# Performance work log

Measured on AMD Instinct MI355X. Metric: run time of the kernel, lower is better.

Reference implementation:

```python
import jax, jax.numpy as jnp
import numpy as np

LN_EPS = 1e-5


def setup_inputs() -> dict:
    key = jax.random.key(0)
    ks = jax.random.split(key, 4)
    B, L, Dm, N = 16, 2048, 512, 64
    return {
        "x": jax.random.normal(ks[0], (B, L, Dm), dtype=jnp.float32),
        "A": jax.random.normal(ks[1], (Dm, N), dtype=jnp.float32),
        "C": jax.random.normal(ks[2], (Dm, N), dtype=jnp.float32),
        "D": jax.random.normal(ks[3], (Dm,), dtype=jnp.float32),
        "gamma": jnp.ones((Dm,), dtype=jnp.float32),
        "beta": jnp.zeros((Dm,), dtype=jnp.float32),
    }


def reference(x, A, C, D, gamma, beta):
    # LayerNorm over last dim (matches nn.LayerNorm(d_model))
    mean = jnp.mean(x, axis=-1, keepdims=True)
    var = jnp.mean(jnp.square(x - mean), axis=-1, keepdims=True)
    x_norm = (x - mean) * jax.lax.rsqrt(var + LN_EPS) * gamma + beta

    B, L, Dm = x.shape
    N = A.shape[1]
    h0 = jnp.zeros((B, N), dtype=x.dtype)

    def step(h, u):
        # u: [B, Dm]; h: [B, N]
        h = jnp.tanh(u @ A + h)
        y = h @ C.T + u * D  # [B, Dm]
        return h, y

    # scan over time: xs [L, B, Dm]
    _, ys = jax.lax.scan(step, h0, jnp.swapaxes(x_norm, 0, 1))
    out = jnp.swapaxes(ys, 0, 1)  # [B, L, Dm]
    return out + x
```

## Files before the change

### kernel.cpp

```cpp
#include <hip/hip_runtime.h>
#include <hip/hip_bf16.h>

typedef short bf16x8 __attribute__((ext_vector_type(8)));
typedef float f32x4 __attribute__((ext_vector_type(4)));

constexpr int B_ = 16;
constexpr int L_ = 2048;
constexpr int DM = 512;
constexpr int NS = 64;
constexpr int BL = B_ * L_;
constexpr float LN_EPS = 1e-5f;
constexpr float KLN = 2.8853900817779268f;

constexpr int SEGS = 32;
constexpr int LSEG = L_ / SEGS;
constexpr int WARM = 64;

__device__ __forceinline__ unsigned f32bits(float f) {
    union { float f; unsigned u; } v{f}; return v.u;
}
__device__ __forceinline__ float bitsf32(unsigned u) {
    union { unsigned u; float f; } v{u}; return v.f;
}
__device__ __forceinline__ unsigned short f2bf(float f) {
    unsigned u = f32bits(f);
    unsigned r = u + 0x7FFF + ((u >> 16) & 1);
    return (unsigned short)(r >> 16);
}

__device__ __forceinline__ void norm_split8(float4 u0, float4 u1,
                                            float rstd, float m2,
                                            bf16x8& ah, bf16x8& al) {
    float t[8] = { fmaf(u0.x, rstd, m2), fmaf(u0.y, rstd, m2),
                   fmaf(u0.z, rstd, m2), fmaf(u0.w, rstd, m2),
                   fmaf(u1.x, rstd, m2), fmaf(u1.y, rstd, m2),
                   fmaf(u1.z, rstd, m2), fmaf(u1.w, rstd, m2) };
    unsigned hb[8], lb[8];
    #pragma unroll
    for (int j = 0; j < 8; ++j) {
        unsigned tb = f32bits(t[j]);
        hb[j] = tb & 0xFFFF0000u;
        lb[j] = f32bits(t[j] - bitsf32(hb[j]));
    }
    union { unsigned u[4]; bf16x8 v; } H, L;
    #pragma unroll
    for (int p = 0; p < 4; ++p) {
        H.u[p] = (hb[2*p] >> 16) | hb[2*p+1];
        L.u[p] = (lb[2*p] >> 16) | (lb[2*p+1] & 0xFFFF0000u);
    }
    ah = H.v; al = L.v;
}

__global__ __launch_bounds__(256) void k_pack(const float* __restrict__ A,
                                              const float* __restrict__ C,
                                              const float* __restrict__ gamma,
                                              const float* __restrict__ beta,
                                              const float* __restrict__ Dv,
                                              unsigned short* __restrict__ PAh,
                                              unsigned short* __restrict__ PAl,
                                              unsigned short* __restrict__ PC,
                                              float* __restrict__ c0,
                                              float* __restrict__ gd,
                                              float* __restrict__ bd) {
    const int blk = blockIdx.x;
    const int tid = threadIdx.x;
    if (blk < 32) {
        const int g = blk * 256 + tid;
        if (g < 4096) {
            const int lane = g & 63, ct = (g >> 6) & 3, k32 = (g >> 8) & 3, kc = g >> 10;
            const int kbase = kc * 128 + k32 * 32 + (lane >> 4) * 8;
            const int col   = ct * 16 + (lane & 15);
            unsigned hb[8], lb[8];
            #pragma unroll
            for (int j = 0; j < 8; ++j) {
                float v = gamma[kbase + j] * A[(size_t)(kbase + j) * NS + col];
                unsigned tb = f32bits(v);
                hb[j] = tb & 0xFFFF0000u;
                lb[j] = f32bits(v - bitsf32(hb[j]));
            }
            uint4 ph, pl;
            ph.x = (hb[0] >> 16) | hb[1]; ph.y = (hb[2] >> 16) | hb[3];
            ph.z = (hb[4] >> 16) | hb[5]; ph.w = (hb[6] >> 16) | hb[7];
            pl.x = (lb[0] >> 16) | (lb[1] & 0xFFFF0000u);
            pl.y = (lb[2] >> 16) | (lb[3] & 0xFFFF0000u);
            pl.z = (lb[4] >> 16) | (lb[5] & 0xFFFF0000u);
            pl.w = (lb[6] >> 16) | (lb[7] & 0xFFFF0000u);
            *reinterpret_cast<uint4*>(PAh + (size_t)g * 8) = ph;
            *reinterpret_cast<uint4*>(PAl + (size_t)g * 8) = pl;
        } else {
            const int g2 = g - 4096;
            const int d = g2 >> 3, s = g2 & 7;
            const int nbase = (s ^ (d & 7)) * 8;
            unsigned short v[8];
            #pragma unroll
            for (int j = 0; j < 8; ++j) v[j] = f2bf(C[(size_t)d * NS + nbase + j]);
            uint4 p;
            p.x = v[0] | ((unsigned)v[1] << 16); p.y = v[2] | ((unsigned)v[3] << 16);
            p.z = v[4] | ((unsigned)v[5] << 16); p.w = v[6] | ((unsigned)v[7] << 16);
            *reinterpret_cast<uint4*>(PC + (size_t)g2 * 8) = p;
        }
    } else {
        __shared__ float red[256];
        #pragma unroll
        for (int i = 0; i < 2; ++i) {
            int d = tid + 256 * i;
            gd[d] = gamma[d] * Dv[d];
            bd[d] = beta[d] * Dv[d];
        }
        const int n = tid & 63, part = tid >> 6;
        float s = 0.f;
        #pragma unroll 8
        for (int k = part * 128; k < part * 128 + 128; ++k)
            s += beta[k] * A[(size_t)k * NS + n];
        red[tid] = s;
        __syncthreads();
        if (tid < 64)
            c0[tid] = red[tid] + red[tid + 64] + red[tid + 128] + red[tid + 192];
    }
}

__global__ __launch_bounds__(256) void k_gemmA(const float* __restrict__ x,
                                               const unsigned short* __restrict__ PAh,
                                               const unsigned short* __restrict__ PAl,
                                               const float* __restrict__ c0,
                                               float* __restrict__ stats,
                                               float* __restrict__ Bu) {
    __shared__ unsigned short AsH[4 * 4 * 64 * 8];
    __shared__ unsigned short AsL[4 * 4 * 64 * 8];
    const int tid  = threadIdx.x;
    const int r0   = blockIdx.x * 64;
    const int w    = tid >> 6;
    const int lane = tid & 63;
    const int myrow = 16 * w + (lane & 15);
    const int kb    = (lane >> 4) * 8;
    const float* xrow = x + (size_t)(r0 + myrow) * DM;

    float s = 0.f, s2 = 0.f;
    #pragma unroll
    for (int kc = 0; kc < 4; ++kc) {
        #pragma unroll
        for (int k32 = 0; k32 < 4; ++k32) {
            float4 a = *reinterpret_cast<const float4*>(xrow + kc * 128 + k32 * 32 + kb);
            float4 b = *reinterpret_cast<const float4*>(xrow + kc * 128 + k32 * 32 + kb + 4);
            s  += (a.x + a.y) + (a.z + a.w) + (b.x + b.y) + (b.z + b.w);
            s2 += a.x*a.x + a.y*a.y + a.z*a.z + a.w*a.w
                + b.x*b.x + b.y*b.y + b.z*b.z + b.w*b.w;
        }
    }
    s += __shfl_xor(s, 16); s2 += __shfl_xor(s2, 16);
    s += __shfl_xor(s, 32); s2 += __shfl_xor(s2, 32);
    const float mean = s * (1.0f / DM);
    const float var  = s2 * (1.0f / DM) - mean * mean;
    const float rstd = rsqrtf(var + LN_EPS);
    const float m2   = -mean * rstd;
    if (lane < 16) {
        stats[2 * (r0 + myrow)]     = mean;
        stats[2 * (r0 + myrow) + 1] = rstd;
    }

    f32x4 acc[4] = {};
    const bf16x8* ABh = reinterpret_cast<const bf16x8*>(AsH);
    const bf16x8* ABl = reinterpret_cast<const bf16x8*>(AsL);

    float4 xv[8];
    #pragma unroll
    for (int k32 = 0; k32 < 4; ++k32) {
        xv[2*k32]   = *reinterpret_cast<const float4*>(xrow + k32 * 32 + kb);
        xv[2*k32+1] = *reinterpret_cast<const float4*>(xrow + k32 * 32 + kb + 4);
    }

    for (int kc = 0; kc < 4; ++kc) {
        {
            const float4* sh = reinterpret_cast<const float4*>(PAh + (size_t)kc * 8192);
            const float4* sl = reinterpret_cast<const float4*>(PAl + (size_t)kc * 8192);
            float4* dh = reinterpret_cast<float4*>(AsH);
            float4* dl = reinterpret_cast<float4*>(AsL);
            #pragma unroll
            for (int i = 0; i < 4; ++i) {
                dh[tid + 256 * i] = sh[tid + 256 * i];
                dl[tid + 256 * i] = sl[tid + 256 * i];
            }
        }
        float4 nxt[8];
        if (kc < 3) {
            #pragma unroll
            for (int k32 = 0; k32 < 4; ++k32) {
                nxt[2*k32]   = *reinterpret_cast<const float4*>(
                    xrow + (kc + 1) * 128 + k32 * 32 + kb);
                nxt[2*k32+1] = *reinterpret_cast<const float4*>(
                    xrow + (kc + 1) * 128 + k32 * 32 + kb + 4);
            }
        }
        __syncthreads();
        #pragma unroll
        for (int k32 = 0; k32 < 4; ++k32) {
            bf16x8 ah, al;
            norm_split8(xv[2*k32], xv[2*k32+1], rstd, m2, ah, al);
            #pragma unroll
            for (int ct = 0; ct < 4; ++ct) {
                bf16x8 bh = ABh[(k32 * 4 + ct) * 64 + lane];
                bf16x8 bl = ABl[(k32 * 4 + ct) * 64 + lane];
                acc[ct] = __builtin_amdgcn_mfma_f32_16x16x32_bf16(ah, bh, acc[ct], 0, 0, 0);
                acc[ct] = __builtin_amdgcn_mfma_f32_16x16x32_bf16(ah, bl, acc[ct], 0, 0, 0);
                acc[ct] = __builtin_amdgcn_mfma_f32_16x16x32_bf16(al, bh, acc[ct], 0, 0, 0);
            }
        }
        __syncthreads();
        if (kc < 3) {
            #pragma unroll
            for (int i = 0; i < 8; ++i) xv[i] = nxt[i];
        }
    }

    const int orow = r0 + 16 * w + (lane >> 4) * 4;
    #pragma unroll
    for (int ct = 0; ct < 4; ++ct) {
        const int n = ct * 16 + (lane & 15);
        const float c0n = c0[n];
        #pragma unroll
        for (int j = 0; j < 4; ++j)
            Bu[(size_t)(orow + j) * NS + n] = acc[ct][j] + c0n;
    }
}

__global__ __launch_bounds__(64) void k_scan(const float* __restrict__ Bu,
                                             unsigned short* __restrict__ h) {
    constexpr int G = 16;
    const int seg = blockIdx.x & (SEGS - 1);
    const int b   = blockIdx.x / SEGS;
    const int n   = threadIdx.x;
    const int l0     = seg * LSEG;
    const int start  = (seg == 0) ? 0 : (l0 - WARM);
    const int nGrp   = (l0 + LSEG - start) / G;
    const int gStore = (l0 - start) / G;

    const float* bp = Bu + (size_t)b * L_ * NS + n;
    unsigned short* hp = h + (size_t)b * L_ * NS + n;

    float bufA[G], bufB[G];
    #pragma unroll
    for (int j = 0; j < G; ++j) bufA[j] = KLN * bp[(size_t)(start + j) * NS];

    float hv = 0.0f;
    int g = 0;
    for (;;) {
        {
            const int base = start + (g + 1) * G;
            if (g + 1 < nGrp) {
                #pragma unroll
                for (int j = 0; j < G; ++j)
                    bufB[j] = KLN * bp[(size_t)(base + j) * NS];
            }
            unsigned short* hq = hp + (size_t)(start + g * G) * NS;
            const bool doStore = g >= gStore;
            #pragma unroll
            for (int j = 0; j < G; ++j) {
                float t = fmaf(hv, KLN, bufA[j]);
                float e = __builtin_amdgcn_exp2f(t);
                float rr = __builtin_amdgcn_rcpf(e + 1.0f);
                hv = fmaf(-2.0f, rr, 1.0f);
                if (doStore) hq[(size_t)j * NS] = f2bf(hv);
            }
        }
        if (++g == nGrp) break;
        {
            const int base = start + (g + 1) * G;
            if (g + 1 < nGrp) {
                #pragma unroll
                for (int j = 0; j < G; ++j)
                    bufA[j] = KLN * bp[(size_t)(base + j) * NS];
            }
            unsigned short* hq = hp + (size_t)(start + g * G) * NS;
            const bool doStore = g >= gStore;
            #pragma unroll
            for (int j = 0; j < G; ++j) {
                float t = fmaf(hv, KLN, bufB[j]);
                float e = __builtin_amdgcn_exp2f(t);
                float rr = __builtin_amdgcn_rcpf(e + 1.0f);
                hv = fmaf(-2.0f, rr, 1.0f);
                if (doStore) hq[(size_t)j * NS] = f2bf(hv);
            }
        }
        if (++g == nGrp) break;
    }
}

__global__ __launch_bounds__(256) void k_gemmC(const float* __restrict__ x,
                                               const unsigned short* __restrict__ PC,
                                               const float* __restrict__ gd,
                                               const float* __restrict__ bd,
                                               const float* __restrict__ stats,
                                               const unsigned short* __restrict__ h,
                                               float* __restrict__ out) {
    __shared__ unsigned short Hs[64 * 64];
    __shared__ unsigned short Cs[128 * 64];
    const int tid  = threadIdx.x;
    const int r0   = (blockIdx.x >> 2) * 64;
    const int d0   = (blockIdx.x & 3) * 128;
    const int w    = tid >> 6;
    const int lane = tid & 63;

    {
        const float4* src = reinterpret_cast<const float4*>(PC + (size_t)d0 * NS);
        float4* dst = reinterpret_cast<float4*>(Cs);
        #pragma unroll
        for (int i = 0; i < 4; ++i) dst[tid + 256 * i] = src[tid + 256 * i];
    }
    {
        const char* hb = reinterpret_cast<const char*>(h + (size_t)r0 * NS);
        #pragma unroll
        for (int it = 0; it < 2; ++it) {
            const int o   = it * 4096 + tid * 16;
            const int row = o >> 7;
            const int s   = (o >> 4) & 7;
            uint4 v = *reinterpret_cast<const uint4*>(hb + row * 128 + ((s ^ (row & 7)) << 4));
            *reinterpret_cast<uint4*>(reinterpret_cast<char*>(Hs) + o) = v;
        }
    }
    __syncthreads();

    f32x4 acc[8] = {};
    const int arow = 16 * w + (lane & 15);
    #pragma unroll
    for (int kt = 0; kt < 2; ++kt) {
        const int c = kt * 4 + (lane >> 4);
        bf16x8 a = *reinterpret_cast<const bf16x8*>(
            reinterpret_cast<char*>(Hs) + arow * 128 + ((c ^ (arow & 7)) << 4));
        #pragma unroll
        for (int ct = 0; ct < 8; ++ct) {
            const int dl = ct * 16 + (lane & 15);
            bf16x8 bfr = *reinterpret_cast<const bf16x8*>(
                reinterpret_cast<char*>(Cs) + dl * 128 + ((c ^ (dl & 7)) << 4));
            acc[ct] = __builtin_amdgcn_mfma_f32_16x16x32_bf16(a, bfr, acc[ct], 0, 0, 0);
        }
    }

    const int rbase = r0 + 16 * w + (lane >> 4) * 4;
    float mean_[4], rstd_[4];
    #pragma unroll
    for (int j = 0; j < 4; ++j) {
        mean_[j] = stats[2 * (rbase + j)];
        rstd_[j] = stats[2 * (rbase + j) + 1];
    }
    #pragma unroll
    for (int ct = 0; ct < 8; ++ct) {
        const int d  = d0 + ct * 16 + (lane & 15);
        const float gdv = gd[d];
        const float bdv = bd[d];
        #pragma unroll
        for (int j = 0; j < 4; ++j) {
            const size_t idx = (size_t)(rbase + j) * DM + d;
            const float xv = x[idx];
            const float z  = (xv - mean_[j]) * rstd_[j];
            out[idx] = acc[ct][j] + z * gdv + bdv + xv;
        }
    }
}

extern "C" void kernel_launch(void* const* d_in, const int* in_sizes, int n_in,
                              void* d_out, int out_size, void* d_ws, size_t ws_size,
                              hipStream_t stream) {
    const float* x     = (const float*)d_in[0];
    const float* A     = (const float*)d_in[1];
    const float* C     = (const float*)d_in[2];
    const float* Dv    = (const float*)d_in[3];
    const float* gamma = (const float*)d_in[4];
    const float* beta  = (const float*)d_in[5];
    float* out = (float*)d_out;

    char* ws = (char*)d_ws;
    float* Bu           = (float*)(ws);
    unsigned short* h   = (unsigned short*)(ws + (size_t)BL * NS * 4);
    float* stats        = (float*)(ws + (size_t)BL * NS * 6);
    char* p = ws + (size_t)BL * NS * 6 + (size_t)BL * 2 * 4;
    unsigned short* PAh = (unsigned short*)p;            p += (size_t)DM * NS * 2;
    unsigned short* PAl = (unsigned short*)p;            p += (size_t)DM * NS * 2;
    unsigned short* PC  = (unsigned short*)p;            p += (size_t)DM * NS * 2;
    float* c0           = (float*)p;                     p += 256;
    float* gd           = (float*)p;                     p += (size_t)DM * 4;
    float* bd           = (float*)p;

    k_pack<<<33, 256, 0, stream>>>(A, C, gamma, beta, Dv, PAh, PAl, PC, c0, gd, bd);
    k_gemmA<<<BL / 64, 256, 0, stream>>>(x, PAh, PAl, c0, stats, Bu);
    k_scan<<<B_ * SEGS, 64, 0, stream>>>(Bu, h);
    k_gemmC<<<(BL / 64) * (DM / 128), 256, 0, stream>>>(x, PC, gd, bd, stats, h, out);
}
```

Measured before the change: 78.00 us.

## Load full projection matrix into LDS once and keep whole x row in registers

The A-projection GEMM kernel now uses 512-thread blocks covering 128 rows. The whole packed hi/lo A matrix (128 KB) is staged in shared memory once up front instead of being reloaded per k-chunk with two barriers each. Each thread also holds its entire row slice of x in registers, so x is read once for both the LayerNorm stats and the MFMA operands rather than twice. This removes redundant global traffic and per-chunk synchronisation, but the large LDS footprint and 128 float registers for x may limit occupancy (launch bounds ask for 2 blocks per CU) and remove any load/compute overlap.

After: 73.75 us. 1.06x faster.

```diff
diff --git a/kernel.cpp b/kernel.cpp
--- a/kernel.cpp
+++ b/kernel.cpp
@@ -119,33 +119,52 @@
     }
 }
 
-__global__ __launch_bounds__(256) void k_gemmA(const float* __restrict__ x,
+__global__ __launch_bounds__(512, 2) void k_gemmA(const float* __restrict__ x,
                                                const unsigned short* __restrict__ PAh,
                                                const unsigned short* __restrict__ PAl,
                                                const float* __restrict__ c0,
                                                float* __restrict__ stats,
                                                float* __restrict__ Bu) {
-    __shared__ unsigned short AsH[4 * 4 * 64 * 8];
-    __shared__ unsigned short AsL[4 * 4 * 64 * 8];
+    __shared__ unsigned short AsH[4 * 16 * 64 * 8];
+    __shared__ unsigned short AsL[4 * 16 * 64 * 8];
     const int tid  = threadIdx.x;
-    const int r0   = blockIdx.x * 64;
+    const int r0   = blockIdx.x * 128;
     const int w    = tid >> 6;
     const int lane = tid & 63;
     const int myrow = 16 * w + (lane & 15);
     const int kb    = (lane >> 4) * 8;
     const float* xrow = x + (size_t)(r0 + myrow) * DM;
 
+    {
+        const float4* sh = reinterpret_cast<const float4*>(PAh);
+        const float4* sl = reinterpret_cast<const float4*>(PAl);
+        float4* dh = reinterpret_cast<float4*>(AsH);
+        float4* dl = reinterpret_cast<float4*>(AsL);
+        #pragma unroll
+        for (int i = 0; i < 8; ++i) {
+            dh[tid + 512 * i] = sh[tid + 512 * i];
+            dl[tid + 512 * i] = sl[tid + 512 * i];
+        }
+    }
+
+    float4 xv[32];
+    #pragma unroll
+    for (int kc = 0; kc < 4; ++kc) {
+        #pragma unroll
+        for (int k32 = 0; k32 < 4; ++k32) {
+            xv[kc * 8 + 2 * k32]     = *reinterpret_cast<const float4*>(
+                xrow + kc * 128 + k32 * 32 + kb);
+            xv[kc * 8 + 2 * k32 + 1] = *reinterpret_cast<const float4*>(
+                xrow + kc * 128 + k32 * 32 + kb + 4);
+        }
+    }
+
     float s = 0.f, s2 = 0.f;
     #pragma unroll
-    for (int kc = 0; kc < 4; ++kc) {
-        #pragma unroll
-        for (int k32 = 0; k32 < 4; ++k32) {
-            float4 a = *reinterpret_cast<const float4*>(xrow + kc * 128 + k32 * 32 + kb);
-            float4 b = *reinterpret_cast<const float4*>(xrow + kc * 128 + k32 * 32 + kb + 4);
-            s  += (a.x + a.y) + (a.z + a.w) + (b.x + b.y) + (b.z + b.w);
-            s2 += a.x*a.x + a.y*a.y + a.z*a.z + a.w*a.w
-                + b.x*b.x + b.y*b.y + b.z*b.z + b.w*b.w;
-        }
+    for (int i = 0; i < 32; ++i) {
+        float4 a = xv[i];
+        s  += (a.x + a.y) + (a.z + a.w);
+        s2 += a.x*a.x + a.y*a.y + a.z*a.z + a.w*a.w;
     }
     s += __shfl_xor(s, 16); s2 += __shfl_xor(s2, 16);
     s += __shfl_xor(s, 32); s2 += __shfl_xor(s2, 32);
@@ -158,57 +177,27 @@
         stats[2 * (r0 + myrow) + 1] = rstd;
     }
 
+    __syncthreads();
+
     f32x4 acc[4] = {};
     const bf16x8* ABh = reinterpret_cast<const bf16x8*>(AsH);
     const bf16x8* ABl = reinterpret_cast<const bf16x8*>(AsL);
 
-    float4 xv[8];
-    #pragma unroll
-    for (int k32 = 0; k32 < 4; ++k32) {
-        xv[2*k32]   = *reinterpret_cast<const float4*>(xrow + k32 * 32 + kb);
-        xv[2*k32+1] = *reinterpret_cast<const float4*>(xrow + k32 * 32 + kb + 4);
-    }
-
+    #pragma unroll
     for (int kc = 0; kc < 4; ++kc) {
-        {
-            const float4* sh = reinterpret_cast<const float4*>(PAh + (size_t)kc * 8192);
-            const float4* sl = reinterpret_cast<const float4*>(PAl + (size_t)kc * 8192);
-            float4* dh = reinterpret_cast<float4*>(AsH);
-            float4* dl = reinterpret_cast<float4*>(AsL);
-            #pragma unroll
-            for (int i = 0; i < 4; ++i) {
-                dh[tid + 256 * i] = sh[tid + 256 * i];
-                dl[tid + 256 * i] = sl[tid + 256 * i];
-            }
-        }
-        float4 nxt[8];
-        if (kc < 3) {
-            #pragma unroll
-            for (int k32 = 0; k32 < 4; ++k32) {
-                nxt[2*k32]   = *reinterpret_cast<const float4*>(
-                    xrow + (kc + 1) * 128 + k32 * 32 + kb);
-                nxt[2*k32+1] = *reinterpret_cast<const float4*>(
-                    xrow + (kc + 1) * 128 + k32 * 32 + kb + 4);
-            }
-        }
-        __syncthreads();
         #pragma unroll
         for (int k32 = 0; k32 < 4; ++k32) {
             bf16x8 ah, al;
-            norm_split8(xv[2*k32], xv[2*k32+1], rstd, m2, ah, al);
+            norm_split8(xv[kc * 8 + 2 * k32], xv[kc * 8 + 2 * k32 + 1], rstd, m2, ah, al);
             #pragma unroll
             for (int ct = 0; ct < 4; ++ct) {
-                bf16x8 bh = ABh[(k32 * 4 + ct) * 64 + lane];
-                bf16x8 bl = ABl[(k32 * 4 + ct) * 64 + lane];
+                const int fi = ((kc * 4 + k32) * 4 + ct) * 64 + lane;
+                bf16x8 bh = ABh[fi];
+                bf16x8 bl = ABl[fi];
                 acc[ct] = __builtin_amdgcn_mfma_f32_16x16x32_bf16(ah, bh, acc[ct], 0, 0, 0);
                 acc[ct] = __builtin_amdgcn_mfma_f32_16x16x32_bf16(ah, bl, acc[ct], 0, 0, 0);
                 acc[ct] = __builtin_amdgcn_mfma_f32_16x16x32_bf16(al, bh, acc[ct], 0, 0, 0);
             }
-        }
-        __syncthreads();
-        if (kc < 3) {
-            #pragma unroll
-            for (int i = 0; i < 8; ++i) xv[i] = nxt[i];
         }
     }
 
@@ -381,7 +370,7 @@
     float* bd           = (float*)p;
 
     k_pack<<<33, 256, 0, stream>>>(A, C, gamma, beta, Dv, PAh, PAl, PC, c0, gd, bd);
-    k_gemmA<<<BL / 64, 256, 0, stream>>>(x, PAh, PAl, c0, stats, Bu);
+    k_gemmA<<<BL / 128, 512, 0, stream>>>(x, PAh, PAl, c0, stats, Bu);
     k_scan<<<B_ * SEGS, 64, 0, stream>>>(Bu, h);
     k_gemmC<<<(BL / 64) * (DM / 128), 256, 0, stream>>>(x, PC, gd, bd, stats, h, out);
 }
```
